# Performance work log

Hardware: AMD Instinct MI355X
Metric: run time of the kernel (lower is better)

## Reference

```python
import jax, jax.numpy as jnp
import numpy as np

B, H, W, C, NH, WS, SHIFT = 32, 56, 56, 128, 4, 7, 3
N = WS * WS            # tokens per window = 49
HD = C // NH           # head dim = 32
HID = int(C * 4.0)     # mlp hidden = 512
SCALE = HD ** -0.5
EPS = 1e-5


def _rel_index():
    coords = np.stack(np.meshgrid(np.arange(WS), np.arange(WS), indexing='ij')).reshape(2, -1)
    rel = (coords[:, :, None] - coords[:, None, :]).transpose(1, 2, 0).copy()
    rel[:, :, 0] += WS - 1
    rel[:, :, 1] += WS - 1
    rel[:, :, 0] *= 2 * WS - 1
    return jnp.asarray(rel.sum(-1), jnp.int32)  # [N, N]


def setup_inputs() -> dict:
    key = jax.random.key(0)
    ks = jax.random.split(key, 8)
    n = lambda k, s, std=0.02: jax.random.normal(k, s, jnp.float32) * std
    return {
        'x': jax.random.normal(ks[0], (B, H * W, C), jnp.float32),
        'attn_mask': jnp.zeros(((H // WS) * (W // WS), N, N), jnp.float32),  # unused (source bug)
        'norm1_w': jnp.ones((C,), jnp.float32), 'norm1_b': jnp.zeros((C,), jnp.float32),
        'qkv_w': n(ks[1], (3 * C, C)), 'qkv_b': jnp.zeros((3 * C,), jnp.float32),
        'rel_table': n(ks[2], ((2 * WS - 1) ** 2, NH)),
        'rel_index': _rel_index(),
        'proj_w': n(ks[3], (C, C)), 'proj_b': jnp.zeros((C,), jnp.float32),
        'norm2_w': jnp.ones((C,), jnp.float32), 'norm2_b': jnp.zeros((C,), jnp.float32),
        'fc1_w': n(ks[4], (HID, C)), 'fc1_b': jnp.zeros((HID,), jnp.float32),
        'fc2_w': n(ks[5], (C, HID)), 'fc2_b': jnp.zeros((C,), jnp.float32),
    }


def _ln(x, w, b):
    m = x.mean(-1, keepdims=True)
    v = jnp.mean((x - m) ** 2, -1, keepdims=True)
    return (x - m) * jax.lax.rsqrt(v + EPS) * w + b


def reference(x, attn_mask, norm1_w, norm1_b, qkv_w, qkv_b, rel_table, rel_index,
              proj_w, proj_b, norm2_w, norm2_b, fc1_w, fc1_b, fc2_w, fc2_b):
    # NOTE: attn_mask is accepted but never used by the source WindowAttention (faithful).
    shortcut = x
    h = _ln(x, norm1_w, norm1_b).reshape(B, H, W, C)
    # cyclic shift (shift_size > 0)
    h = jnp.roll(h, (-SHIFT, -SHIFT), axis=(1, 2))
    # window partition -> [B*nW, N, C]
    h = h.reshape(B, H // WS, WS, W // WS, WS, C).transpose(0, 1, 3, 2, 4, 5).reshape(-1, N, C)
    # window attention
    qkv = (h @ qkv_w.T + qkv_b).reshape(-1, N, 3, NH, HD)
    q = qkv[:, :, 0].transpose(0, 2, 1, 3)  # [BW, NH, N, HD]
    k = qkv[:, :, 1].transpose(0, 2, 1, 3)
    v = qkv[:, :, 2].transpose(0, 2, 1, 3)
    attn = jnp.einsum('whnd,whmd->whnm', q, k) * SCALE  # [BW, NH, N, N]
    bias = rel_table[rel_index.reshape(-1)].reshape(N, N, NH).transpose(2, 0, 1)
    attn = jax.nn.softmax(attn + bias[None], axis=-1)
    out = jnp.einsum('whnm,whmd->whnd', attn, v).transpose(0, 2, 1, 3).reshape(-1, N, C)
    out = out @ proj_w.T + proj_b
    # window reverse -> [B, H, W, C]
    out = out.reshape(B, H // WS, W // WS, WS, WS, C).transpose(0, 1, 3, 2, 4, 5).reshape(B, H, W, C)
    out = jnp.roll(out, (SHIFT, SHIFT), axis=(1, 2)).reshape(B, H * W, C)
    y = shortcut + out
    # MLP block
    h2 = _ln(y, norm2_w, norm2_b)
    h2 = jax.nn.gelu(h2 @ fc1_w.T + fc1_b, approximate=False)
    h2 = h2 @ fc2_w.T + fc2_b
    return y + h2
```

## Files before the change

### kernel.cpp

```cpp
#include <hip/hip_runtime.h>

typedef __bf16 bf16;
typedef __bf16 bf16x4 __attribute__((ext_vector_type(4)));
typedef __bf16 bf16x8 __attribute__((ext_vector_type(8)));
typedef float f32x4 __attribute__((ext_vector_type(4)));

#define NTOK 49
#define HW 56
#define SHIFT3 3
constexpr float kScale = 0.17677669529663687f;

#define WS_BIAS  0
#define WS_QKVW  50176
#define WS_PROJW 148480
#define WS_FC1W  181248
#define WS_FC2W  312320

static __device__ __forceinline__ f32x4 mfma16(bf16x8 a, bf16x8 b, f32x4 c) {
    return __builtin_amdgcn_mfma_f32_16x16x32_bf16(a, b, c, 0, 0, 0);
}

static __device__ __forceinline__ float gelu_f(float x) {
    float x2 = x * x;
    float u2 = x * (1.5957691216f + 0.0713548162f * x2);
    return x / (1.0f + __expf(-u2));
}


__global__ void bias_kernel(const float* __restrict__ rel_table,
                            const int* __restrict__ rel_index,
                            float* __restrict__ biasbuf) {
    int idx = blockIdx.x * 256 + threadIdx.x;
    if (idx >= 4 * NTOK * 64) return;
    int j = idx & 63;
    int rest = idx >> 6;
    int i = rest % NTOK;
    int h = rest / NTOK;
    float v = -1e30f;
    if (j < NTOK) v = rel_table[rel_index[i * NTOK + j] * 4 + h];
    biasbuf[idx] = v;
}

__global__ void wcvt_kernel(const float* __restrict__ qkv_w, const float* __restrict__ proj_w,
                            const float* __restrict__ fc1_w, const float* __restrict__ fc2_w,
                            bf16* __restrict__ qkvwp, bf16* __restrict__ projwp,
                            bf16* __restrict__ fc1wp, bf16* __restrict__ fc2wp) {
    int idx = blockIdx.x * 256 + threadIdx.x;
    if (idx < 49152) {
        int o = idx, e = o & 7, t = o >> 3, g = t & 3; t >>= 2;
        int row = t % 384, ks = t / 384;
        qkvwp[o] = (bf16)qkv_w[row * 128 + ks * 32 + g * 8 + e];
    } else if (idx < 65536) {
        int o = idx - 49152, e = o & 7, t = o >> 3, g = t & 3; t >>= 2;
        int row = t % 128, ks = t / 128;
        projwp[o] = (bf16)proj_w[row * 128 + ks * 32 + g * 8 + e];
    } else if (idx < 131072) {
        int o = idx - 65536, e = o & 7, t = o >> 3, g = t & 3; t >>= 2;
        int row = t % 512, ks = t / 512;
        fc1wp[o] = (bf16)fc1_w[row * 128 + ks * 32 + g * 8 + e];
    } else {
        int o = idx - 131072, e = o & 7, t = o >> 3, g = t & 3; t >>= 2;
        int row = t % 128, ks = t / 128;
        fc2wp[o] = (bf16)fc2_w[row * 512 + ks * 32 + g * 8 + e];
    }
}


__global__ __launch_bounds__(256, 2) void attn_kernel(
    const float* __restrict__ x,
    const float* __restrict__ n1w, const float* __restrict__ n1b,
    const bf16*  __restrict__ qkvwp, const float* __restrict__ qkv_b,
    const bf16*  __restrict__ projwp, const float* __restrict__ proj_b,
    const float* __restrict__ biasbuf,
    float* __restrict__ yout)
{
    __shared__ __align__(16) char smem[65536];
    bf16* const hb = (bf16*)smem;

    const int tid  = threadIdx.x;
    const int wave = tid >> 6;
    const int lane = tid & 63;
    const int g = lane >> 4;
    const int c = lane & 15;

    char* const qbase  = smem + 16384 + wave * 8192;
    char* const kbase  = qbase + 4096;
    char* const pbase  = qbase;
    char* const vtbase = smem + 49152 + wave * 4096;

    const int w  = blockIdx.x;
    const int b  = w >> 6;
    const int wi = (w >> 3) & 7;
    const int wj = w & 7;
    const int head = wave;

    {
        const int slot = tid >> 5, l32 = tid & 31;
        for (int it = 0; it < 8; ++it) {
            int t  = slot + (it << 3);
            int tt = t < NTOK ? t : NTOK - 1;
            int r  = tt / 7, cc = tt - r * 7;
            int row = wi * 7 + r + SHIFT3;  if (row >= HW) row -= HW;
            int col = wj * 7 + cc + SHIFT3; if (col >= HW) col -= HW;
            const float* src = x + (((size_t)(b * 3136 + row * 56 + col)) << 7) + (l32 << 2);
            float4 v = *(const float4*)src;
            float s  = v.x + v.y + v.z + v.w;
            float s2 = v.x * v.x + v.y * v.y + v.z * v.z + v.w * v.w;
            for (int m = 1; m <= 16; m <<= 1) {
                s  += __shfl_xor(s,  m, 64);
                s2 += __shfl_xor(s2, m, 64);
            }
            float mean = s * (1.0f / 128.0f);
            float var  = s2 * (1.0f / 128.0f) - mean * mean;
            float rs   = rsqrtf(var + 1e-5f);
            float4 wv = *(const float4*)(n1w + (l32 << 2));
            float4 bv = *(const float4*)(n1b + (l32 << 2));
            bf16x4 outv;
            if (t < NTOK) {
                outv[0] = (bf16)((v.x - mean) * rs * wv.x + bv.x);
                outv[1] = (bf16)((v.y - mean) * rs * wv.y + bv.y);
                outv[2] = (bf16)((v.z - mean) * rs * wv.z + bv.z);
                outv[3] = (bf16)((v.w - mean) * rs * wv.w + bv.w);
            } else {
                outv[0] = (bf16)0.0f; outv[1] = (bf16)0.0f;
                outv[2] = (bf16)0.0f; outv[3] = (bf16)0.0f;
            }
            int off = (l32 << 3) ^ ((t & 7) << 4);
            *(bf16x4*)((char*)hb + t * 256 + off) = outv;
        }
    }
    __syncthreads();

    f32x4 fz = {0.f, 0.f, 0.f, 0.f};
    #pragma unroll 1
    for (int nt = 0; nt < 2; ++nt) {
        f32x4 qa[4], ka[4], va[4];
        #pragma unroll
        for (int mt = 0; mt < 4; ++mt) { qa[mt] = fz; ka[mt] = fz; va[mt] = fz; }

        #pragma unroll
        for (int ks = 0; ks < 4; ++ks) {
            bf16x8 af[4];
            const int koff = ks * 64 + g * 16;
            #pragma unroll
            for (int mt = 0; mt < 4; ++mt) {
                int row = mt * 16 + c;
                af[mt] = *(const bf16x8*)((char*)hb + row * 256 + (koff ^ ((row & 7) << 4)));
            }
            int jb = head * 32 + nt * 16 + c;
            bf16x8 bq = *(const bf16x8*)(qkvwp + (((ks * 384 + jb) * 4 + g) << 3));
            bf16x8 bk = *(const bf16x8*)(qkvwp + (((ks * 384 + 128 + jb) * 4 + g) << 3));
            bf16x8 bv = *(const bf16x8*)(qkvwp + (((ks * 384 + 256 + jb) * 4 + g) << 3));
            #pragma unroll
            for (int mt = 0; mt < 4; ++mt) {
                qa[mt] = mfma16(af[mt], bq, qa[mt]);
                ka[mt] = mfma16(af[mt], bk, ka[mt]);
                va[mt] = mfma16(af[mt], bv, va[mt]);
            }
        }
        int dl = nt * 16 + c;
        float bqs = qkv_b[head * 32 + dl];
        float bks = qkv_b[128 + head * 32 + dl];
        float bvs = qkv_b[256 + head * 32 + dl];
        #pragma unroll
        for (int mt = 0; mt < 4; ++mt)
            #pragma unroll
            for (int r = 0; r < 4; ++r) {
                int tok = mt * 16 + g * 4 + r;
                *(bf16*)(qbase + tok * 64 + ((dl * 2) ^ ((tok & 3) << 4))) = (bf16)(qa[mt][r] + bqs);
                *(bf16*)(kbase + tok * 64 + ((dl * 2) ^ ((tok & 3) << 4))) = (bf16)(ka[mt][r] + bks);
                *(bf16*)(vtbase + dl * 128 + ((tok * 2) ^ ((dl & 7) << 4))) = (bf16)(va[mt][r] + bvs);
            }
    }
    __syncthreads();

    f32x4 s[4][4];
    for (int mt = 0; mt < 4; ++mt) for (int nt = 0; nt < 4; ++nt) s[mt][nt] = fz;
    {
        bf16x8 aq[4];
        #pragma unroll
        for (int mt = 0; mt < 4; ++mt) {
            int row = mt * 16 + c;
            aq[mt] = *(const bf16x8*)(qbase + row * 64 + ((g * 16) ^ ((row & 3) << 4)));
        }
        #pragma unroll
        for (int nt = 0; nt < 4; ++nt) {
            int row = nt * 16 + c;
            bf16x8 bk = *(const bf16x8*)(kbase + row * 64 + ((g * 16) ^ ((row & 3) << 4)));
            #pragma unroll
            for (int mt = 0; mt < 4; ++mt) s[mt][nt] = mfma16(aq[mt], bk, s[mt][nt]);
        }
    }

    const float* bbase = biasbuf + head * (NTOK * 64);
    float lsum[4][4];
    for (int mt = 0; mt < 4; ++mt) {
        for (int r = 0; r < 4; ++r) {
            int i  = mt * 16 + g * 4 + r;
            int im = i < NTOK ? i : NTOK - 1;
            const float* brow = bbase + im * 64 + c;
            float sv[4];
            float mx = -3e38f;
            for (int nt = 0; nt < 4; ++nt) {
                float val = s[mt][nt][r] * kScale + brow[nt * 16];
                sv[nt] = val;
                mx = fmaxf(mx, val);
            }
            for (int m2 = 1; m2 <= 8; m2 <<= 1) mx = fmaxf(mx, __shfl_xor(mx, m2, 64));
            float sum = 0.f;
            for (int nt = 0; nt < 4; ++nt) {
                float p = __expf(sv[nt] - mx);
                sum += p;
                int jj = nt * 16 + c;
                *(bf16*)(pbase + i * 128 + ((jj * 2) ^ ((i & 7) << 4))) = (bf16)p;
            }
            for (int m2 = 1; m2 <= 8; m2 <<= 1) sum += __shfl_xor(sum, m2, 64);
            lsum[mt][r] = sum;
        }
    }

    f32x4 o[4][2];
    for (int mt = 0; mt < 4; ++mt) for (int nt = 0; nt < 2; ++nt) o[mt][nt] = fz;
    #pragma unroll
    for (int ks = 0; ks < 2; ++ks) {
        bf16x8 ap[4];
        #pragma unroll
        for (int mt = 0; mt < 4; ++mt) {
            int row = mt * 16 + c;
            ap[mt] = *(const bf16x8*)(pbase + row * 128 + ((ks * 64 + g * 16) ^ ((row & 7) << 4)));
        }
        #pragma unroll
        for (int nt = 0; nt < 2; ++nt) {
            int dd = nt * 16 + c;
            bf16x8 bv = *(const bf16x8*)(vtbase + dd * 128 + ((ks * 64 + g * 16) ^ ((dd & 7) << 4)));
            #pragma unroll
            for (int mt = 0; mt < 4; ++mt) o[mt][nt] = mfma16(ap[mt], bv, o[mt][nt]);
        }
    }
    for (int mt = 0; mt < 4; ++mt)
        for (int r = 0; r < 4; ++r) {
            int i = mt * 16 + g * 4 + r;
            if (i < NTOK) {
                float inv = 1.0f / lsum[mt][r];
                for (int nt = 0; nt < 2; ++nt) {
                    int col = head * 32 + nt * 16 + c;
                    *(bf16*)((char*)hb + i * 256 + ((col * 2) ^ ((i & 7) << 4))) = (bf16)(o[mt][nt][r] * inv);
                }
            }
        }
    __syncthreads();

    f32x4 pj[4][2];
    for (int mt = 0; mt < 4; ++mt) for (int nt = 0; nt < 2; ++nt) pj[mt][nt] = fz;
    #pragma unroll
    for (int ks = 0; ks < 4; ++ks) {
        bf16x8 af[4];
        int koff = ks * 64 + g * 16;
        #pragma unroll
        for (int mt = 0; mt < 4; ++mt) {
            int row = mt * 16 + c;
            af[mt] = *(const bf16x8*)((char*)hb + row * 256 + (koff ^ ((row & 7) << 4)));
        }
        #pragma unroll
        for (int nt = 0; nt < 2; ++nt) {
            int colw = wave * 32 + nt * 16 + c;
            bf16x8 bp = *(const bf16x8*)(projwp + (((ks * 128 + colw) * 4 + g) << 3));
            #pragma unroll
            for (int mt = 0; mt < 4; ++mt) pj[mt][nt] = mfma16(af[mt], bp, pj[mt][nt]);
        }
    }
    float pb0 = proj_b[wave * 32 + c];
    float pb1 = proj_b[wave * 32 + 16 + c];
    for (int mt = 0; mt < 4; ++mt)
        for (int r = 0; r < 4; ++r) {
            int i = mt * 16 + g * 4 + r;
            if (i < NTOK) {
                int rr = i / 7, cc = i - rr * 7;
                int row = wi * 7 + rr + SHIFT3;  if (row >= HW) row -= HW;
                int col = wj * 7 + cc + SHIFT3;  if (col >= HW) col -= HW;
                size_t base = ((size_t)(b * 3136 + row * 56 + col)) << 7;
                int c0 = wave * 32 + c;
                yout[base + c0]      = x[base + c0]      + pj[mt][0][r] + pb0;
                yout[base + c0 + 16] = x[base + c0 + 16] + pj[mt][1][r] + pb1;
            }
        }
}


__global__ __launch_bounds__(256, 2) void mlp_kernel(
    const float* __restrict__ n2w, const float* __restrict__ n2b,
    const bf16*  __restrict__ fc1wp, const float* __restrict__ fc1_b,
    const bf16*  __restrict__ fc2wp, const float* __restrict__ fc2_b,
    float* __restrict__ y)
{
    __shared__ __align__(16) char smem[81920];
    bf16* const h2    = (bf16*)smem;
    char* const abase = smem + 16384;

    const int tid  = threadIdx.x;
    const int wave = tid >> 6;
    const int lane = tid & 63;
    const int g = lane >> 4;
    const int c = lane & 15;
    const size_t t0 = (size_t)blockIdx.x * 64;

    {
        const int slot = tid >> 5, l32 = tid & 31;
        for (int it = 0; it < 8; ++it) {
            int t = slot + (it << 3);
            const float* src = y + ((t0 + t) << 7) + (l32 << 2);
            float4 v = *(const float4*)src;
            float s  = v.x + v.y + v.z + v.w;
            float s2 = v.x * v.x + v.y * v.y + v.z * v.z + v.w * v.w;
            for (int m = 1; m <= 16; m <<= 1) {
                s  += __shfl_xor(s,  m, 64);
                s2 += __shfl_xor(s2, m, 64);
            }
            float mean = s * (1.0f / 128.0f);
            float var  = s2 * (1.0f / 128.0f) - mean * mean;
            float rs   = rsqrtf(var + 1e-5f);
            float4 wv = *(const float4*)(n2w + (l32 << 2));
            float4 bv = *(const float4*)(n2b + (l32 << 2));
            bf16x4 outv;
            outv[0] = (bf16)((v.x - mean) * rs * wv.x + bv.x);
            outv[1] = (bf16)((v.y - mean) * rs * wv.y + bv.y);
            outv[2] = (bf16)((v.z - mean) * rs * wv.z + bv.z);
            outv[3] = (bf16)((v.w - mean) * rs * wv.w + bv.w);
            int off = (l32 << 3) ^ ((t & 7) << 4);
            *(bf16x4*)((char*)h2 + t * 256 + off) = outv;
        }
    }
    __syncthreads();

    f32x4 fz = {0.f, 0.f, 0.f, 0.f};
    #pragma unroll 1
    for (int half = 0; half < 2; ++half) {
        f32x4 a1[4][4];
        #pragma unroll
        for (int mt = 0; mt < 4; ++mt) for (int nt = 0; nt < 4; ++nt) a1[mt][nt] = fz;
        #pragma unroll
        for (int ks = 0; ks < 4; ++ks) {
            bf16x8 af[4];
            int koff = ks * 64 + g * 16;
            #pragma unroll
            for (int mt = 0; mt < 4; ++mt) {
                int row = mt * 16 + c;
                af[mt] = *(const bf16x8*)((char*)h2 + row * 256 + (koff ^ ((row & 7) << 4)));
            }
            #pragma unroll
            for (int nt = 0; nt < 4; ++nt) {
                int col = wave * 128 + half * 64 + nt * 16 + c;
                bf16x8 bw = *(const bf16x8*)(fc1wp + (((ks * 512 + col) * 4 + g) << 3));
                #pragma unroll
                for (int mt = 0; mt < 4; ++mt) a1[mt][nt] = mfma16(af[mt], bw, a1[mt][nt]);
            }
        }
        #pragma unroll
        for (int nt = 0; nt < 4; ++nt) {
            int col = wave * 128 + half * 64 + nt * 16 + c;
            float fb = fc1_b[col];
            #pragma unroll
            for (int mt = 0; mt < 4; ++mt)
                #pragma unroll
                for (int r = 0; r < 4; ++r) {
                    int row = mt * 16 + g * 4 + r;
                    float ge = gelu_f(a1[mt][nt][r] + fb);
                    *(bf16*)(abase + row * 1024 + ((col * 2) ^ ((row & 7) << 4))) = (bf16)ge;
                }
        }
    }
    __syncthreads();

    f32x4 a2[4][2];
    for (int mt = 0; mt < 4; ++mt) for (int nt = 0; nt < 2; ++nt) a2[mt][nt] = fz;
    #pragma unroll 1
    for (int ks = 0; ks < 16; ++ks) {
        bf16x8 af[4];
        int koff = ks * 64 + g * 16;
        #pragma unroll
        for (int mt = 0; mt < 4; ++mt) {
            int row = mt * 16 + c;
            af[mt] = *(const bf16x8*)(abase + row * 1024 + (koff ^ ((row & 7) << 4)));
        }
        #pragma unroll
        for (int nt = 0; nt < 2; ++nt) {
            int col = wave * 32 + nt * 16 + c;
            bf16x8 bw = *(const bf16x8*)(fc2wp + (((ks * 128 + col) * 4 + g) << 3));
            #pragma unroll
            for (int mt = 0; mt < 4; ++mt) a2[mt][nt] = mfma16(af[mt], bw, a2[mt][nt]);
        }
    }
    for (int nt = 0; nt < 2; ++nt) {
        int col = wave * 32 + nt * 16 + c;
        float fb = fc2_b[col];
        for (int mt = 0; mt < 4; ++mt)
            for (int r = 0; r < 4; ++r) {
                int row = mt * 16 + g * 4 + r;
                size_t idx = ((t0 + row) << 7) + col;
                y[idx] = y[idx] + a2[mt][nt][r] + fb;
            }
    }
}


extern "C" void kernel_launch(void* const* d_in, const int* in_sizes, int n_in,
                              void* d_out, int out_size, void* d_ws, size_t ws_size,
                              hipStream_t stream) {
    const float* x        = (const float*)d_in[0];
    const float* n1w      = (const float*)d_in[2];
    const float* n1b      = (const float*)d_in[3];
    const float* qkv_w    = (const float*)d_in[4];
    const float* qkv_b    = (const float*)d_in[5];
    const float* rel_tab  = (const float*)d_in[6];
    const int*   rel_idx  = (const int*)d_in[7];
    const float* proj_w   = (const float*)d_in[8];
    const float* proj_b   = (const float*)d_in[9];
    const float* n2w      = (const float*)d_in[10];
    const float* n2b      = (const float*)d_in[11];
    const float* fc1_w    = (const float*)d_in[12];
    const float* fc1_b    = (const float*)d_in[13];
    const float* fc2_w    = (const float*)d_in[14];
    const float* fc2_b    = (const float*)d_in[15];

    float* yout = (float*)d_out;
    char*  ws   = (char*)d_ws;
    float* biasbuf = (float*)(ws + WS_BIAS);
    bf16*  qkvwp = (bf16*)(ws + WS_QKVW);
    bf16*  projwp= (bf16*)(ws + WS_PROJW);
    bf16*  fc1wp = (bf16*)(ws + WS_FC1W);
    bf16*  fc2wp = (bf16*)(ws + WS_FC2W);

    bias_kernel<<<dim3(49), dim3(256), 0, stream>>>(rel_tab, rel_idx, biasbuf);
    wcvt_kernel<<<dim3(768), dim3(256), 0, stream>>>(qkv_w, proj_w, fc1_w, fc2_w,
                                                     qkvwp, projwp, fc1wp, fc2wp);
    attn_kernel<<<dim3(2048), dim3(256), 0, stream>>>(x, n1w, n1b, qkvwp, qkv_b,
                                                      projwp, proj_b, biasbuf, yout);
    mlp_kernel<<<dim3(1568), dim3(256), 0, stream>>>(n2w, n2b, fc1wp, fc1_b,
                                                     fc2wp, fc2_b, yout);
}
```

Baseline: 277.4 us.

## Transpose MFMA operands for vectorized epilogues and shrink MLP tile to 32 tokens

Swaps the A/B operands of the MFMAs so each lane holds four consecutive output columns. The Q/K/V, P, attention-output and projection epilogues can then use bf16x4 and float4 stores and loads instead of scalar ones, and the softmax row reduction needs only two cross-lane shuffles. The MLP kernel now processes 32 tokens per block with 32KB of shared memory, reusing the LDS region for the GELU activations. It raises launch bounds to 4 blocks per SM and doubles the grid, for more occupancy and coalesced residual updates. The cost is less weight reuse per block and a heavier fc1 register tile.

After: 257.7 us. 1.08x faster.

```diff
diff --git a/kernel.cpp b/kernel.cpp
--- a/kernel.cpp
+++ b/kernel.cpp
@@ -153,104 +153,129 @@
             bf16x8 bv = *(const bf16x8*)(qkvwp + (((ks * 384 + 256 + jb) * 4 + g) << 3));
             #pragma unroll
             for (int mt = 0; mt < 4; ++mt) {
-                qa[mt] = mfma16(af[mt], bq, qa[mt]);
-                ka[mt] = mfma16(af[mt], bk, ka[mt]);
+                qa[mt] = mfma16(bq, af[mt], qa[mt]);
+                ka[mt] = mfma16(bk, af[mt], ka[mt]);
                 va[mt] = mfma16(af[mt], bv, va[mt]);
             }
         }
-        int dl = nt * 16 + c;
-        float bqs = qkv_b[head * 32 + dl];
-        float bks = qkv_b[128 + head * 32 + dl];
-        float bvs = qkv_b[256 + head * 32 + dl];
-        #pragma unroll
-        for (int mt = 0; mt < 4; ++mt)
+        f32x4 qb4 = *(const f32x4*)(qkv_b + head * 32 + nt * 16 + g * 4);
+        f32x4 kb4 = *(const f32x4*)(qkv_b + 128 + head * 32 + nt * 16 + g * 4);
+        float vb  = qkv_b[256 + head * 32 + nt * 16 + c];
+        #pragma unroll
+        for (int mt = 0; mt < 4; ++mt) {
+            int tok = mt * 16 + c;
+            bf16x4 qv, kv;
             #pragma unroll
             for (int r = 0; r < 4; ++r) {
-                int tok = mt * 16 + g * 4 + r;
-                *(bf16*)(qbase + tok * 64 + ((dl * 2) ^ ((tok & 3) << 4))) = (bf16)(qa[mt][r] + bqs);
-                *(bf16*)(kbase + tok * 64 + ((dl * 2) ^ ((tok & 3) << 4))) = (bf16)(ka[mt][r] + bks);
-                *(bf16*)(vtbase + dl * 128 + ((tok * 2) ^ ((dl & 7) << 4))) = (bf16)(va[mt][r] + bvs);
-            }
+                qv[r] = (bf16)(qa[mt][r] + qb4[r]);
+                kv[r] = (bf16)(ka[mt][r] + kb4[r]);
+            }
+            int qoff = (nt * 32 + g * 8) ^ ((tok & 3) << 4);
+            *(bf16x4*)(qbase + tok * 64 + qoff) = qv;
+            *(bf16x4*)(kbase + tok * 64 + qoff) = kv;
+            int dl = nt * 16 + c;
+            bf16x4 vv;
+            #pragma unroll
+            for (int r = 0; r < 4; ++r) vv[r] = (bf16)(va[mt][r] + vb);
+            *(bf16x4*)(vtbase + dl * 128 + ((mt * 32 + g * 8) ^ ((dl & 7) << 4))) = vv;
+        }
     }
     __syncthreads();
 
     f32x4 s[4][4];
-    for (int mt = 0; mt < 4; ++mt) for (int nt = 0; nt < 4; ++nt) s[mt][nt] = fz;
+    #pragma unroll
+    for (int bm = 0; bm < 4; ++bm) for (int bn = 0; bn < 4; ++bn) s[bm][bn] = fz;
     {
         bf16x8 aq[4];
         #pragma unroll
-        for (int mt = 0; mt < 4; ++mt) {
-            int row = mt * 16 + c;
-            aq[mt] = *(const bf16x8*)(qbase + row * 64 + ((g * 16) ^ ((row & 3) << 4)));
-        }
-        #pragma unroll
-        for (int nt = 0; nt < 4; ++nt) {
-            int row = nt * 16 + c;
-            bf16x8 bk = *(const bf16x8*)(kbase + row * 64 + ((g * 16) ^ ((row & 3) << 4)));
-            #pragma unroll
-            for (int mt = 0; mt < 4; ++mt) s[mt][nt] = mfma16(aq[mt], bk, s[mt][nt]);
+        for (int bm = 0; bm < 4; ++bm) {
+            int row = bm * 16 + c;
+            aq[bm] = *(const bf16x8*)(qbase + row * 64 + ((g * 16) ^ ((row & 3) << 4)));
+        }
+        #pragma unroll
+        for (int bn = 0; bn < 4; ++bn) {
+            int row = bn * 16 + c;
+            bf16x8 kf = *(const bf16x8*)(kbase + row * 64 + ((g * 16) ^ ((row & 3) << 4)));
+            #pragma unroll
+            for (int bm = 0; bm < 4; ++bm) s[bm][bn] = mfma16(kf, aq[bm], s[bm][bn]);
         }
     }
 
     const float* bbase = biasbuf + head * (NTOK * 64);
-    float lsum[4][4];
+    float linv[4];
+    #pragma unroll
+    for (int bm = 0; bm < 4; ++bm) {
+        int qt = bm * 16 + c;
+        int im = qt < NTOK ? qt : NTOK - 1;
+        const float* brow = bbase + im * 64;
+        f32x4 vals[4];
+        float mx = -3e38f;
+        #pragma unroll
+        for (int bn = 0; bn < 4; ++bn) {
+            f32x4 b4 = *(const f32x4*)(brow + bn * 16 + g * 4);
+            #pragma unroll
+            for (int r = 0; r < 4; ++r) {
+                float v = s[bm][bn][r] * kScale + b4[r];
+                vals[bn][r] = v;
+                mx = fmaxf(mx, v);
+            }
+        }
+        mx = fmaxf(mx, __shfl_xor(mx, 16, 64));
+        mx = fmaxf(mx, __shfl_xor(mx, 32, 64));
+        float sum = 0.f;
+        #pragma unroll
+        for (int bn = 0; bn < 4; ++bn) {
+            bf16x4 pv;
+            #pragma unroll
+            for (int r = 0; r < 4; ++r) {
+                float p = __expf(vals[bn][r] - mx);
+                sum += p;
+                pv[r] = (bf16)p;
+            }
+            *(bf16x4*)(pbase + qt * 128 + ((bn * 32 + g * 8) ^ ((c & 7) << 4))) = pv;
+        }
+        sum += __shfl_xor(sum, 16, 64);
+        sum += __shfl_xor(sum, 32, 64);
+        linv[bm] = 1.0f / sum;
+    }
+
+    f32x4 o[4][2];
+    #pragma unroll
+    for (int mt = 0; mt < 4; ++mt) for (int nt = 0; nt < 2; ++nt) o[mt][nt] = fz;
+    #pragma unroll
+    for (int ks = 0; ks < 2; ++ks) {
+        int koff = ks * 64 + g * 16;
+        bf16x8 vf[2], pf[4];
+        #pragma unroll
+        for (int nt = 0; nt < 2; ++nt)
+            vf[nt] = *(const bf16x8*)(vtbase + (nt * 16 + c) * 128 + (koff ^ ((c & 7) << 4)));
+        #pragma unroll
+        for (int mt = 0; mt < 4; ++mt)
+            pf[mt] = *(const bf16x8*)(pbase + (mt * 16 + c) * 128 + (koff ^ ((c & 7) << 4)));
+        #pragma unroll
+        for (int mt = 0; mt < 4; ++mt)
+            #pragma unroll
+            for (int nt = 0; nt < 2; ++nt) o[mt][nt] = mfma16(vf[nt], pf[mt], o[mt][nt]);
+    }
+    #pragma unroll
     for (int mt = 0; mt < 4; ++mt) {
-        for (int r = 0; r < 4; ++r) {
-            int i  = mt * 16 + g * 4 + r;
-            int im = i < NTOK ? i : NTOK - 1;
-            const float* brow = bbase + im * 64 + c;
-            float sv[4];
-            float mx = -3e38f;
-            for (int nt = 0; nt < 4; ++nt) {
-                float val = s[mt][nt][r] * kScale + brow[nt * 16];
-                sv[nt] = val;
-                mx = fmaxf(mx, val);
-            }
-            for (int m2 = 1; m2 <= 8; m2 <<= 1) mx = fmaxf(mx, __shfl_xor(mx, m2, 64));
-            float sum = 0.f;
-            for (int nt = 0; nt < 4; ++nt) {
-                float p = __expf(sv[nt] - mx);
-                sum += p;
-                int jj = nt * 16 + c;
-                *(bf16*)(pbase + i * 128 + ((jj * 2) ^ ((i & 7) << 4))) = (bf16)p;
-            }
-            for (int m2 = 1; m2 <= 8; m2 <<= 1) sum += __shfl_xor(sum, m2, 64);
-            lsum[mt][r] = sum;
-        }
-    }
-
-    f32x4 o[4][2];
-    for (int mt = 0; mt < 4; ++mt) for (int nt = 0; nt < 2; ++nt) o[mt][nt] = fz;
-    #pragma unroll
-    for (int ks = 0; ks < 2; ++ks) {
-        bf16x8 ap[4];
-        #pragma unroll
-        for (int mt = 0; mt < 4; ++mt) {
-            int row = mt * 16 + c;
-            ap[mt] = *(const bf16x8*)(pbase + row * 128 + ((ks * 64 + g * 16) ^ ((row & 7) << 4)));
-        }
-        #pragma unroll
-        for (int nt = 0; nt < 2; ++nt) {
-            int dd = nt * 16 + c;
-            bf16x8 bv = *(const bf16x8*)(vtbase + dd * 128 + ((ks * 64 + g * 16) ^ ((dd & 7) << 4)));
-            #pragma unroll
-            for (int mt = 0; mt < 4; ++mt) o[mt][nt] = mfma16(ap[mt], bv, o[mt][nt]);
-        }
-    }
-    for (int mt = 0; mt < 4; ++mt)
-        for (int r = 0; r < 4; ++r) {
-            int i = mt * 16 + g * 4 + r;
-            if (i < NTOK) {
-                float inv = 1.0f / lsum[mt][r];
-                for (int nt = 0; nt < 2; ++nt) {
-                    int col = head * 32 + nt * 16 + c;
-                    *(bf16*)((char*)hb + i * 256 + ((col * 2) ^ ((i & 7) << 4))) = (bf16)(o[mt][nt][r] * inv);
-                }
-            }
-        }
+        int qt = mt * 16 + c;
+        if (qt < NTOK) {
+            float inv = linv[mt];
+            #pragma unroll
+            for (int nt = 0; nt < 2; ++nt) {
+                bf16x4 ov;
+                #pragma unroll
+                for (int r = 0; r < 4; ++r) ov[r] = (bf16)(o[mt][nt][r] * inv);
+                int coff = (head * 64 + nt * 32 + g * 8) ^ ((qt & 7) << 4);
+                *(bf16x4*)((char*)hb + qt * 256 + coff) = ov;
+            }
+        }
+    }
     __syncthreads();
 
     f32x4 pj[4][2];
+    #pragma unroll
     for (int mt = 0; mt < 4; ++mt) for (int nt = 0; nt < 2; ++nt) pj[mt][nt] = fz;
     #pragma unroll
     for (int ks = 0; ks < 4; ++ks) {
@@ -266,47 +291,51 @@
             int colw = wave * 32 + nt * 16 + c;
             bf16x8 bp = *(const bf16x8*)(projwp + (((ks * 128 + colw) * 4 + g) << 3));
             #pragma unroll
-            for (int mt = 0; mt < 4; ++mt) pj[mt][nt] = mfma16(af[mt], bp, pj[mt][nt]);
-        }
-    }
-    float pb0 = proj_b[wave * 32 + c];
-    float pb1 = proj_b[wave * 32 + 16 + c];
-    for (int mt = 0; mt < 4; ++mt)
-        for (int r = 0; r < 4; ++r) {
-            int i = mt * 16 + g * 4 + r;
-            if (i < NTOK) {
-                int rr = i / 7, cc = i - rr * 7;
-                int row = wi * 7 + rr + SHIFT3;  if (row >= HW) row -= HW;
-                int col = wj * 7 + cc + SHIFT3;  if (col >= HW) col -= HW;
-                size_t base = ((size_t)(b * 3136 + row * 56 + col)) << 7;
-                int c0 = wave * 32 + c;
-                yout[base + c0]      = x[base + c0]      + pj[mt][0][r] + pb0;
-                yout[base + c0 + 16] = x[base + c0 + 16] + pj[mt][1][r] + pb1;
-            }
-        }
-}
-
-
-__global__ __launch_bounds__(256, 2) void mlp_kernel(
+            for (int mt = 0; mt < 4; ++mt) pj[mt][nt] = mfma16(bp, af[mt], pj[mt][nt]);
+        }
+    }
+    f32x4 pb0 = *(const f32x4*)(proj_b + wave * 32 + g * 4);
+    f32x4 pb1 = *(const f32x4*)(proj_b + wave * 32 + 16 + g * 4);
+    #pragma unroll
+    for (int mt = 0; mt < 4; ++mt) {
+        int qt = mt * 16 + c;
+        if (qt < NTOK) {
+            int rr = qt / 7, cc = qt - rr * 7;
+            int row = wi * 7 + rr + SHIFT3;  if (row >= HW) row -= HW;
+            int col = wj * 7 + cc + SHIFT3;  if (col >= HW) col -= HW;
+            size_t base = ((size_t)(b * 3136 + row * 56 + col)) << 7;
+            int c0 = wave * 32 + g * 4;
+            f32x4 x0 = *(const f32x4*)(x + base + c0);
+            f32x4 x1 = *(const f32x4*)(x + base + c0 + 16);
+            f32x4 y0 = x0 + pj[mt][0] + pb0;
+            f32x4 y1 = x1 + pj[mt][1] + pb1;
+            *(f32x4*)(yout + base + c0)      = y0;
+            *(f32x4*)(yout + base + c0 + 16) = y1;
+        }
+    }
+}
+
+
+__global__ __launch_bounds__(256, 4) void mlp_kernel(
     const float* __restrict__ n2w, const float* __restrict__ n2b,
     const bf16*  __restrict__ fc1wp, const float* __restrict__ fc1_b,
     const bf16*  __restrict__ fc2wp, const float* __restrict__ fc2_b,
     float* __restrict__ y)
 {
-    __shared__ __align__(16) char smem[81920];
+    __shared__ __align__(16) char smem[32768];
     bf16* const h2    = (bf16*)smem;
-    char* const abase = smem + 16384;
+    char* const abase = smem;
 
     const int tid  = threadIdx.x;
     const int wave = tid >> 6;
     const int lane = tid & 63;
     const int g = lane >> 4;
     const int c = lane & 15;
-    const size_t t0 = (size_t)blockIdx.x * 64;
+    const size_t t0 = (size_t)blockIdx.x * 32;
 
     {
         const int slot = tid >> 5, l32 = tid & 31;
-        for (int it = 0; it < 8; ++it) {
+        for (int it = 0; it < 4; ++it) {
             int t = slot + (it << 3);
             const float* src = y + ((t0 + t) << 7) + (l32 << 2);
             float4 v = *(const float4*)src;
@@ -333,52 +362,52 @@
     __syncthreads();
 
     f32x4 fz = {0.f, 0.f, 0.f, 0.f};
-    #pragma unroll 1
-    for (int half = 0; half < 2; ++half) {
-        f32x4 a1[4][4];
-        #pragma unroll
-        for (int mt = 0; mt < 4; ++mt) for (int nt = 0; nt < 4; ++nt) a1[mt][nt] = fz;
-        #pragma unroll
-        for (int ks = 0; ks < 4; ++ks) {
-            bf16x8 af[4];
-            int koff = ks * 64 + g * 16;
-            #pragma unroll
-            for (int mt = 0; mt < 4; ++mt) {
-                int row = mt * 16 + c;
-                af[mt] = *(const bf16x8*)((char*)h2 + row * 256 + (koff ^ ((row & 7) << 4)));
-            }
-            #pragma unroll
-            for (int nt = 0; nt < 4; ++nt) {
-                int col = wave * 128 + half * 64 + nt * 16 + c;
-                bf16x8 bw = *(const bf16x8*)(fc1wp + (((ks * 512 + col) * 4 + g) << 3));
-                #pragma unroll
-                for (int mt = 0; mt < 4; ++mt) a1[mt][nt] = mfma16(af[mt], bw, a1[mt][nt]);
-            }
-        }
-        #pragma unroll
-        for (int nt = 0; nt < 4; ++nt) {
-            int col = wave * 128 + half * 64 + nt * 16 + c;
-            float fb = fc1_b[col];
-            #pragma unroll
-            for (int mt = 0; mt < 4; ++mt)
-                #pragma unroll
-                for (int r = 0; r < 4; ++r) {
-                    int row = mt * 16 + g * 4 + r;
-                    float ge = gelu_f(a1[mt][nt][r] + fb);
-                    *(bf16*)(abase + row * 1024 + ((col * 2) ^ ((row & 7) << 4))) = (bf16)ge;
-                }
-        }
-    }
-    __syncthreads();
-
-    f32x4 a2[4][2];
-    for (int mt = 0; mt < 4; ++mt) for (int nt = 0; nt < 2; ++nt) a2[mt][nt] = fz;
-    #pragma unroll 1
+    f32x4 a1[8][2];
+    #pragma unroll
+    for (int nt = 0; nt < 8; ++nt) for (int mt = 0; mt < 2; ++mt) a1[nt][mt] = fz;
+    #pragma unroll
+    for (int ks = 0; ks < 4; ++ks) {
+        bf16x8 af[2];
+        int koff = ks * 64 + g * 16;
+        #pragma unroll
+        for (int mt = 0; mt < 2; ++mt) {
+            int row = mt * 16 + c;
+            af[mt] = *(const bf16x8*)((char*)h2 + row * 256 + (koff ^ ((row & 7) << 4)));
+        }
+        #pragma unroll
+        for (int nt = 0; nt < 8; ++nt) {
+            int col = wave * 128 + nt * 16 + c;
+            bf16x8 bw = *(const bf16x8*)(fc1wp + (((ks * 512 + col) * 4 + g) << 3));
+            #pragma unroll
+            for (int mt = 0; mt < 2; ++mt) a1[nt][mt] = mfma16(bw, af[mt], a1[nt][mt]);
+        }
+    }
+    __syncthreads();
+
+    #pragma unroll
+    for (int nt = 0; nt < 8; ++nt) {
+        f32x4 fb4 = *(const f32x4*)(fc1_b + wave * 128 + nt * 16 + g * 4);
+        #pragma unroll
+        for (int mt = 0; mt < 2; ++mt) {
+            int tok = mt * 16 + c;
+            bf16x4 gv;
+            #pragma unroll
+            for (int r = 0; r < 4; ++r) gv[r] = (bf16)gelu_f(a1[nt][mt][r] + fb4[r]);
+            int coff = (wave * 256 + nt * 32 + g * 8) ^ ((tok & 7) << 4);
+            *(bf16x4*)(abase + tok * 1024 + coff) = gv;
+        }
+    }
+    __syncthreads();
+
+    f32x4 a2[2][2];
+    #pragma unroll
+    for (int nt = 0; nt < 2; ++nt) for (int mt = 0; mt < 2; ++mt) a2[nt][mt] = fz;
+    #pragma unroll 4
     for (int ks = 0; ks < 16; ++ks) {
-        bf16x8 af[4];
+        bf16x8 af[2];
         int koff = ks * 64 + g * 16;
         #pragma unroll
-        for (int mt = 0; mt < 4; ++mt) {
+        for (int mt = 0; mt < 2; ++mt) {
             int row = mt * 16 + c;
             af[mt] = *(const bf16x8*)(abase + row * 1024 + (koff ^ ((row & 7) << 4)));
         }
@@ -387,18 +416,19 @@
             int col = wave * 32 + nt * 16 + c;
             bf16x8 bw = *(const bf16x8*)(fc2wp + (((ks * 128 + col) * 4 + g) << 3));
             #pragma unroll
-            for (int mt = 0; mt < 4; ++mt) a2[mt][nt] = mfma16(af[mt], bw, a2[mt][nt]);
-        }
-    }
+            for (int mt = 0; mt < 2; ++mt) a2[nt][mt] = mfma16(bw, af[mt], a2[nt][mt]);
+        }
+    }
+    #pragma unroll
     for (int nt = 0; nt < 2; ++nt) {
-        int col = wave * 32 + nt * 16 + c;
-        float fb = fc2_b[col];
-        for (int mt = 0; mt < 4; ++mt)
-            for (int r = 0; r < 4; ++r) {
-                int row = mt * 16 + g * 4 + r;
-                size_t idx = ((t0 + row) << 7) + col;
-                y[idx] = y[idx] + a2[mt][nt][r] + fb;
-            }
+        f32x4 fb4 = *(const f32x4*)(fc2_b + wave * 32 + nt * 16 + g * 4);
+        #pragma unroll
+        for (int mt = 0; mt < 2; ++mt) {
+            size_t idx = ((t0 + mt * 16 + c) << 7) + wave * 32 + nt * 16 + g * 4;
+            f32x4 yv = *(const f32x4*)(y + idx);
+            yv = yv + a2[nt][mt] + fb4;
+            *(f32x4*)(y + idx) = yv;
+        }
     }
 }
 
@@ -435,6 +465,6 @@
                                                      qkvwp, projwp, fc1wp, fc2wp);
     attn_kernel<<<dim3(2048), dim3(256), 0, stream>>>(x, n1w, n1b, qkvwp, qkv_b,
                                                       projwp, proj_b, biasbuf, yout);
-    mlp_kernel<<<dim3(1568), dim3(256), 0, stream>>>(n2w, n2b, fc1wp, fc1_b,
+    mlp_kernel<<<dim3(3136), dim3(256), 0, stream>>>(n2w, n2b, fc1wp, fc1_b,
                                                      fc2wp, fc2_b, yout);
 }
```
